# Performance work log

Measured on AMD Instinct MI355X. Metric: run time of the kernel, lower is better.

## Reference

```python
import jax, jax.numpy as jnp
import numpy as np

TEMP_UPDATE = 1e-05
EPS = 1e-12  # torch F.normalize eps


def _l2norm(x, axis):
    n = jnp.sqrt(jnp.sum(x * x, axis=axis, keepdims=True))
    return x / jnp.maximum(n, EPS)


def setup_inputs() -> dict:
    key = jax.random.key(0)
    k1, k2 = jax.random.split(key)
    query = jax.random.normal(k1, (64, 256, 512), dtype=jnp.float32)
    keys = jax.random.normal(k2, (2048, 512), dtype=jnp.float32)
    return {"query": query, "keys": keys}


def reference(query, keys):
    bs, t, d = query.shape
    m = keys.shape[0]
    # F.normalize(query, dim=2)
    q = _l2norm(query, axis=2)
    qr = q.reshape(bs * t, d)                      # [N, d]
    score = qr @ keys.T                            # [N, m]
    score_query = jax.nn.softmax(score, axis=0)    # softmax over queries per slot
    score_memory = jax.nn.softmax(score, axis=1)   # softmax over slots per query
    # topk(1) over memory dim -> argmax slot per query
    g = jnp.argmax(score_memory, axis=1)           # [N] int
    col_max = jnp.max(score_query, axis=0)         # [m]
    # weight per query: score_query[n, g_n] / max(score_query[:, g_n])
    w = jnp.take_along_axis(score_query, g[:, None], axis=1)[:, 0] / col_max[g]
    # fused scatter-add replacing the per-slot python loop
    query_update = jax.ops.segment_sum(w[:, None] * qr, g, num_segments=m)  # [m, d]
    updated = _l2norm(TEMP_UPDATE * query_update + keys, axis=1)
    return jax.lax.stop_gradient(updated)  # original returns .detach()
```

## Files before the change

kernel.cpp:

```cpp
#include <hip/hip_runtime.h>
#include <math.h>

#define N_Q     16384
#define DDIM    512
#define M_SLOTS 2048
#define EPSN    1e-12f
#define TEMPU   1e-5f
#define KSCALE  25.4f
#define QSCALE  127.0f
#define INV_S   (1.0f / (127.0f * 25.4f))
#define NZBLK   73
#define BCAP    32

typedef unsigned int u32;
typedef unsigned long long u64;
typedef __attribute__((ext_vector_type(4))) int i32x4;

__device__ __forceinline__ void gld_lds16(const void* g, void* l) {
    __builtin_amdgcn_global_load_lds(
        (const __attribute__((address_space(1))) u32*)(g),
        (__attribute__((address_space(3))) u32*)(l), 16, 0, 0);
}
__device__ __forceinline__ float block_reduce_sum_128(float v, float* sred, int t) {
    #pragma unroll
    for (int o = 32; o > 0; o >>= 1) v += __shfl_down(v, o, 64);
    if ((t & 63) == 0) sred[t >> 6] = v;
    __syncthreads();
    return sred[0] + sred[1];
}
__device__ __forceinline__ char q8(float x, float s) {
    int v = __float2int_rn(x * s);
    v = v < -127 ? -127 : (v > 127 ? 127 : v);
    return (char)v;
}

__global__ __launch_bounds__(128) void k_prep(const float* __restrict__ q,
                                              const float* __restrict__ keys,
                                              char* __restrict__ qi8,
                                              char* __restrict__ ki8,
                                              float4* __restrict__ zbase) {
    __shared__ float sred[2];
    int b = blockIdx.x;
    int t = threadIdx.x;
    if (b < N_Q) {
        float4 v = ((const float4*)(q + (size_t)b * DDIM))[t];
        float ss = v.x * v.x + v.y * v.y + v.z * v.z + v.w * v.w;
        ss = block_reduce_sum_128(ss, sred, t);
        float s = QSCALE / fmaxf(sqrtf(ss), EPSN);
        char4 o;
        o.x = q8(v.x, s);
        o.y = q8(v.y, s);
        o.z = q8(v.z, s);
        o.w = q8(v.w, s);
        ((char4*)(qi8 + (size_t)b * DDIM))[t] = o;
    } else if (b < N_Q + M_SLOTS) {
        int r = b - N_Q;
        float4 v = ((const float4*)(keys + (size_t)r * DDIM))[t];
        char4 o;
        o.x = q8(v.x, KSCALE);
        o.y = q8(v.y, KSCALE);
        o.z = q8(v.z, KSCALE);
        o.w = q8(v.w, KSCALE);
        ((char4*)(ki8 + (size_t)r * DDIM))[t] = o;
    } else {
        int idx = (b - (N_Q + M_SLOTS)) * 128 + t;
        zbase[idx] = make_float4(0.f, 0.f, 0.f, 0.f);
    }
}

__global__ __launch_bounds__(256) void k_score(const char* __restrict__ qi8,
                                               const char* __restrict__ ki8,
                                               u64* __restrict__ rowpack,
                                               u32* __restrict__ colmax) {
    __shared__ char sA[3][128 * 64];
    __shared__ char sB[3][128 * 64];

    int t = threadIdx.x;
    int lane = t & 63;
    int wid = t >> 6;
    int wrow = wid >> 1;
    int wcol = wid & 1;
    int lr = lane & 15;
    int kc = lane >> 4;

    int n0 = blockIdx.y * 128;
    int j0 = blockIdx.x * 128;

    int srow = t >> 2;
    int scolB = (t & 3) * 16;

    const char* gA0 = qi8 + (size_t)(n0 + srow) * DDIM + scolB;
    const char* gA1 = qi8 + (size_t)(n0 + 64 + srow) * DDIM + scolB;
    const char* gB0 = ki8 + (size_t)(j0 + srow) * DDIM + scolB;
    const char* gB1 = ki8 + (size_t)(j0 + 64 + srow) * DDIM + scolB;

    i32x4 acc[4][4] = {};

#define STAGE(buf, k0)  do {                                   \
        gld_lds16(gA0 + (k0), &sA[buf][t * 16]);               \
        gld_lds16(gA1 + (k0), &sA[buf][4096 + t * 16]);        \
        gld_lds16(gB0 + (k0), &sB[buf][t * 16]);               \
        gld_lds16(gB1 + (k0), &sB[buf][4096 + t * 16]);        \
    } while (0)

    STAGE(0, 0);
    STAGE(1, 64);
    asm volatile("s_waitcnt vmcnt(4)" ::: "memory");
    __builtin_amdgcn_s_barrier();
    __builtin_amdgcn_sched_barrier(0);

    #pragma unroll
    for (int kt = 0; kt < 8; ++kt) {
        const int cur = kt % 3;
        if (kt < 6) STAGE((kt + 2) % 3, (kt + 2) * 64);

        i32x4 a[4], b[4];
        #pragma unroll
        for (int i = 0; i < 4; ++i)
            a[i] = *(const i32x4*)&sA[cur][(wrow * 64 + i * 16 + lr) * 64 + kc * 16];
        #pragma unroll
        for (int j = 0; j < 4; ++j)
            b[j] = *(const i32x4*)&sB[cur][(wcol * 64 + j * 16 + lr) * 64 + kc * 16];
        #pragma unroll
        for (int i = 0; i < 4; ++i)
            #pragma unroll
            for (int j = 0; j < 4; ++j)
                acc[i][j] = __builtin_amdgcn_mfma_i32_16x16x64_i8(a[i], b[j], acc[i][j], 0, 0, 0);

        if (kt < 6)       asm volatile("s_waitcnt vmcnt(4)" ::: "memory");
        else if (kt == 6) asm volatile("s_waitcnt vmcnt(0)" ::: "memory");
        if (kt < 7) {
            __builtin_amdgcn_s_barrier();
            __builtin_amdgcn_sched_barrier(0);
        }
    }
#undef STAGE

    #pragma unroll
    for (int i = 0; i < 4; ++i) {
        #pragma unroll
        for (int r = 0; r < 4; ++r) {
            int v = acc[i][0][r];
            int c = j0 + wcol * 64 + lr;
            #pragma unroll
            for (int j = 1; j < 4; ++j) {
                int vj = acc[i][j][r];
                int cj = j0 + wcol * 64 + j * 16 + lr;
                if (vj > v) { v = vj; c = cj; }
            }
            #pragma unroll
            for (int off = 1; off < 16; off <<= 1) {
                int ov = __shfl_xor(v, off, 64);
                int oc = __shfl_xor(c, off, 64);
                if (ov > v || (ov == v && oc < c)) { v = ov; c = oc; }
            }
            if (lr == 0) {
                int grow = n0 + wrow * 64 + i * 16 + kc * 4 + r;
                u64 pk = ((u64)(u32)(v ^ 0x80000000) << 32) | (u64)(~(u32)c);
                atomicMax(rowpack + grow, pk);
            }
        }
    }
    #pragma unroll
    for (int j = 0; j < 4; ++j) {
        int m = acc[0][j][0];
        #pragma unroll
        for (int i = 0; i < 4; ++i)
            #pragma unroll
            for (int r = 0; r < 4; ++r) m = max(m, acc[i][j][r]);
        m = max(m, __shfl_xor(m, 16, 64));
        m = max(m, __shfl_xor(m, 32, 64));
        if (kc == 0) atomicMax(colmax + j0 + wcol * 64 + j * 16 + lr,
                               (u32)m ^ 0x80000000u);
    }
}

__global__ __launch_bounds__(256) void k_fill(const u64* __restrict__ rowpack,
                                              const u32* __restrict__ colmax,
                                              u32* __restrict__ cur,
                                              u32* __restrict__ bperm,
                                              float* __restrict__ bw,
                                              u32* __restrict__ ovf_cnt,
                                              u32* __restrict__ ovf_n,
                                              float* __restrict__ ovf_w) {
    int n = blockIdx.x * 256 + threadIdx.x;
    u64 p = rowpack[n];
    int vi = (int)(((u32)(p >> 32)) ^ 0x80000000u);
    int g = (int)(~(u32)(p & 0xFFFFFFFFull));
    int cm = (int)(colmax[g] ^ 0x80000000u);
    float w = expf((float)(vi - cm) * INV_S);
    u32 pos = atomicAdd(cur + g, 1u);
    if (pos < BCAP) {
        bperm[g * BCAP + pos] = (u32)n;
        bw[g * BCAP + pos] = w;
    } else {
        u32 o = atomicAdd(ovf_cnt, 1u);
        ovf_n[o] = ((u32)g << 16) | (u32)n;
        ovf_w[o] = w;
    }
}

__global__ __launch_bounds__(128) void k_gather_final(const char* __restrict__ qi8,
                                                      const u32* __restrict__ cur,
                                                      const u32* __restrict__ bperm,
                                                      const float* __restrict__ bw,
                                                      const u32* __restrict__ ovf_cnt,
                                                      const u32* __restrict__ ovf_n,
                                                      const float* __restrict__ ovf_w,
                                                      const float* __restrict__ keys,
                                                      float* __restrict__ out) {
    __shared__ float sred[2];
    int j = blockIdx.x;
    int t = threadIdx.x;
    u32 c = cur[j];
    u32 cnt = c < BCAP ? c : BCAP;
    float ax = 0.f, ay = 0.f, az = 0.f, aw = 0.f;
    for (u32 i = 0; i < cnt; ++i) {
        u32 n = bperm[j * BCAP + i];
        float wq = bw[j * BCAP + i] * (1.0f / 127.0f);
        char4 q4 = ((const char4*)(qi8 + (size_t)n * DDIM))[t];
        ax = fmaf(wq, (float)q4.x, ax);
        ay = fmaf(wq, (float)q4.y, ay);
        az = fmaf(wq, (float)q4.z, az);
        aw = fmaf(wq, (float)q4.w, aw);
    }
    if (c > BCAP) {
        u32 oc = *ovf_cnt;
        for (u32 i = 0; i < oc; ++i) {
            u32 e = ovf_n[i];
            if ((e >> 16) == (u32)j) {
                u32 n = e & 0xFFFFu;
                float wq = ovf_w[i] * (1.0f / 127.0f);
                char4 q4 = ((const char4*)(qi8 + (size_t)n * DDIM))[t];
                ax = fmaf(wq, (float)q4.x, ax);
                ay = fmaf(wq, (float)q4.y, ay);
                az = fmaf(wq, (float)q4.z, az);
                aw = fmaf(wq, (float)q4.w, aw);
            }
        }
    }
    float4 k4 = ((const float4*)(keys + (size_t)j * DDIM))[t];
    float4 v;
    v.x = fmaf(TEMPU, ax, k4.x);
    v.y = fmaf(TEMPU, ay, k4.y);
    v.z = fmaf(TEMPU, az, k4.z);
    v.w = fmaf(TEMPU, aw, k4.w);
    float ss = v.x * v.x + v.y * v.y + v.z * v.z + v.w * v.w;
    ss = block_reduce_sum_128(ss, sred, t);
    float inv = 1.0f / fmaxf(sqrtf(ss), EPSN);
    v.x *= inv; v.y *= inv; v.z *= inv; v.w *= inv;
    ((float4*)(out + (size_t)j * DDIM))[t] = v;
}

extern "C" void kernel_launch(void* const* d_in, const int* in_sizes, int n_in,
                              void* d_out, int out_size, void* d_ws, size_t ws_size,
                              hipStream_t stream) {
    const float* query = (const float*)d_in[0];
    const float* keys  = (const float*)d_in[1];
    float* out = (float*)d_out;

    char* ws = (char*)d_ws;
    const size_t OFF_QI8   = 0;
    const size_t OFF_ROW   = 8388608;
    const size_t OFF_CMAX  = OFF_ROW + 131072;
    const size_t OFF_CUR   = OFF_CMAX + 8192;
    const size_t OFF_OVFC  = OFF_CUR + 8192;
    const size_t OFF_BPERM = OFF_OVFC + 2048;
    const size_t OFF_BW    = OFF_BPERM + 262144;
    const size_t OFF_OVFN  = OFF_BW + 262144;
    const size_t OFF_OVFW  = OFF_OVFN + 65536;
    const size_t OFF_KI8   = OFF_OVFW + 65536;

    char*   qi8    = ws + OFF_QI8;
    u64*    rowpack= (u64*)(ws + OFF_ROW);
    u32*    cmax   = (u32*)(ws + OFF_CMAX);
    u32*    cur    = (u32*)(ws + OFF_CUR);
    u32*    ovfc   = (u32*)(ws + OFF_OVFC);
    u32*    bperm  = (u32*)(ws + OFF_BPERM);
    float*  bw     = (float*)(ws + OFF_BW);
    u32*    ovfn   = (u32*)(ws + OFF_OVFN);
    float*  ovfw   = (float*)(ws + OFF_OVFW);
    char*   ki8    = ws + OFF_KI8;

    k_prep<<<N_Q + M_SLOTS + NZBLK, 128, 0, stream>>>(query, keys, qi8, ki8,
                                                      (float4*)(ws + OFF_ROW));

    dim3 g2(M_SLOTS / 128, N_Q / 128);
    k_score<<<g2, 256, 0, stream>>>(qi8, ki8, rowpack, cmax);

    k_fill<<<N_Q / 256, 256, 0, stream>>>(rowpack, cmax, cur, bperm, bw,
                                          ovfc, ovfn, ovfw);
    k_gather_final<<<M_SLOTS, 128, 0, stream>>>(qi8, cur, bperm, bw,
                                                ovfc, ovfn, ovfw, keys, out);
}
```

Baseline: 72.19 us.

## Fuse slot bucketing into score kernel via per-row completion counters

```diff
diff --git a/kernel.cpp b/kernel.cpp
--- a/kernel.cpp
+++ b/kernel.cpp
@@ -9,8 +9,9 @@
 #define KSCALE  25.4f
 #define QSCALE  127.0f
 #define INV_S   (1.0f / (127.0f * 25.4f))
-#define NZBLK   73
 #define BCAP    32
+#define NROWB   4608
+#define NZF     13440
 
 typedef unsigned int u32;
 typedef unsigned long long u64;
@@ -34,44 +35,50 @@
     return (char)v;
 }
 
-__global__ __launch_bounds__(128) void k_prep(const float* __restrict__ q,
+__global__ __launch_bounds__(256) void k_prep(const float* __restrict__ q,
                                               const float* __restrict__ keys,
                                               char* __restrict__ qi8,
                                               char* __restrict__ ki8,
                                               float4* __restrict__ zbase) {
-    __shared__ float sred[2];
     int b = blockIdx.x;
     int t = threadIdx.x;
-    if (b < N_Q) {
-        float4 v = ((const float4*)(q + (size_t)b * DDIM))[t];
-        float ss = v.x * v.x + v.y * v.y + v.z * v.z + v.w * v.w;
-        ss = block_reduce_sum_128(ss, sred, t);
-        float s = QSCALE / fmaxf(sqrtf(ss), EPSN);
-        char4 o;
-        o.x = q8(v.x, s);
-        o.y = q8(v.y, s);
-        o.z = q8(v.z, s);
-        o.w = q8(v.w, s);
-        ((char4*)(qi8 + (size_t)b * DDIM))[t] = o;
-    } else if (b < N_Q + M_SLOTS) {
-        int r = b - N_Q;
-        float4 v = ((const float4*)(keys + (size_t)r * DDIM))[t];
-        char4 o;
-        o.x = q8(v.x, KSCALE);
-        o.y = q8(v.y, KSCALE);
-        o.z = q8(v.z, KSCALE);
-        o.w = q8(v.w, KSCALE);
-        ((char4*)(ki8 + (size_t)r * DDIM))[t] = o;
+    if (b < NROWB) {
+        int lane = t & 63;
+        int row = b * 4 + (t >> 6);
+        bool isq = row < N_Q;
+        const float* src = isq ? q + (size_t)row * DDIM
+                               : keys + (size_t)(row - N_Q) * DDIM;
+        float4 v0 = ((const float4*)src)[lane];
+        float4 v1 = ((const float4*)src)[lane + 64];
+        float ss = v0.x * v0.x + v0.y * v0.y + v0.z * v0.z + v0.w * v0.w
+                 + v1.x * v1.x + v1.y * v1.y + v1.z * v1.z + v1.w * v1.w;
+        #pragma unroll
+        for (int o = 32; o > 0; o >>= 1) ss += __shfl_xor(ss, o, 64);
+        float s = isq ? QSCALE / fmaxf(sqrtf(ss), EPSN) : KSCALE;
+        char4 o0, o1;
+        o0.x = q8(v0.x, s); o0.y = q8(v0.y, s); o0.z = q8(v0.z, s); o0.w = q8(v0.w, s);
+        o1.x = q8(v1.x, s); o1.y = q8(v1.y, s); o1.z = q8(v1.z, s); o1.w = q8(v1.w, s);
+        char* dst = isq ? qi8 + (size_t)row * DDIM
+                        : ki8 + (size_t)(row - N_Q) * DDIM;
+        ((char4*)dst)[lane] = o0;
+        ((char4*)dst)[lane + 64] = o1;
     } else {
-        int idx = (b - (N_Q + M_SLOTS)) * 128 + t;
-        zbase[idx] = make_float4(0.f, 0.f, 0.f, 0.f);
+        int idx = (b - NROWB) * 256 + t;
+        if (idx < NZF) zbase[idx] = make_float4(0.f, 0.f, 0.f, 0.f);
     }
 }
 
 __global__ __launch_bounds__(256) void k_score(const char* __restrict__ qi8,
                                                const char* __restrict__ ki8,
                                                u64* __restrict__ rowpack,
-                                               u32* __restrict__ colmax) {
+                                               u32* __restrict__ colmax,
+                                               u32* __restrict__ done,
+                                               u32* __restrict__ cur,
+                                               u32* __restrict__ bperm,
+                                               int* __restrict__ bvi,
+                                               u32* __restrict__ ovf_cnt,
+                                               u32* __restrict__ ovf_n,
+                                               int* __restrict__ ovf_vi) {
     __shared__ char sA[3][128 * 64];
     __shared__ char sB[3][128 * 64];
 
@@ -111,16 +118,16 @@
 
     #pragma unroll
     for (int kt = 0; kt < 8; ++kt) {
-        const int cur = kt % 3;
+        const int cb = kt % 3;
         if (kt < 6) STAGE((kt + 2) % 3, (kt + 2) * 64);
 
         i32x4 a[4], b[4];
         #pragma unroll
         for (int i = 0; i < 4; ++i)
-            a[i] = *(const i32x4*)&sA[cur][(wrow * 64 + i * 16 + lr) * 64 + kc * 16];
+            a[i] = *(const i32x4*)&sA[cb][(wrow * 64 + i * 16 + lr) * 64 + kc * 16];
         #pragma unroll
         for (int j = 0; j < 4; ++j)
-            b[j] = *(const i32x4*)&sB[cur][(wcol * 64 + j * 16 + lr) * 64 + kc * 16];
+            b[j] = *(const i32x4*)&sB[cb][(wcol * 64 + j * 16 + lr) * 64 + kc * 16];
         #pragma unroll
         for (int i = 0; i < 4; ++i)
             #pragma unroll
@@ -173,51 +180,55 @@
         if (kc == 0) atomicMax(colmax + j0 + wcol * 64 + j * 16 + lr,
                                (u32)m ^ 0x80000000u);
     }
-}
-
-__global__ __launch_bounds__(256) void k_fill(const u64* __restrict__ rowpack,
-                                              const u32* __restrict__ colmax,
-                                              u32* __restrict__ cur,
-                                              u32* __restrict__ bperm,
-                                              float* __restrict__ bw,
-                                              u32* __restrict__ ovf_cnt,
-                                              u32* __restrict__ ovf_n,
-                                              float* __restrict__ ovf_w) {
-    int n = blockIdx.x * 256 + threadIdx.x;
-    u64 p = rowpack[n];
-    int vi = (int)(((u32)(p >> 32)) ^ 0x80000000u);
-    int g = (int)(~(u32)(p & 0xFFFFFFFFull));
-    int cm = (int)(colmax[g] ^ 0x80000000u);
-    float w = expf((float)(vi - cm) * INV_S);
-    u32 pos = atomicAdd(cur + g, 1u);
-    if (pos < BCAP) {
-        bperm[g * BCAP + pos] = (u32)n;
-        bw[g * BCAP + pos] = w;
-    } else {
-        u32 o = atomicAdd(ovf_cnt, 1u);
-        ovf_n[o] = ((u32)g << 16) | (u32)n;
-        ovf_w[o] = w;
+
+    if (lr == 0) {
+        __threadfence();
+        #pragma unroll
+        for (int i = 0; i < 4; ++i) {
+            #pragma unroll
+            for (int r = 0; r < 4; ++r) {
+                int grow = n0 + wrow * 64 + i * 16 + kc * 4 + r;
+                u32 d = atomicAdd(done + grow, 1u);
+                if (d == 15u) {
+                    __threadfence();
+                    u64 p = atomicMax(rowpack + grow, 0ull);
+                    int vi = (int)(((u32)(p >> 32)) ^ 0x80000000u);
+                    int g  = (int)(~(u32)(p & 0xFFFFFFFFull));
+                    u32 pos = atomicAdd(cur + g, 1u);
+                    if (pos < BCAP) {
+                        bperm[g * BCAP + pos] = (u32)grow;
+                        bvi[g * BCAP + pos] = vi;
+                    } else {
+                        u32 o = atomicAdd(ovf_cnt, 1u);
+                        ovf_n[o] = ((u32)g << 16) | (u32)grow;
+                        ovf_vi[o] = vi;
+                    }
+                }
+            }
+        }
     }
 }
 
 __global__ __launch_bounds__(128) void k_gather_final(const char* __restrict__ qi8,
+                                                      const u32* __restrict__ colmax,
                                                       const u32* __restrict__ cur,
                                                       const u32* __restrict__ bperm,
-                                                      const float* __restrict__ bw,
+                                                      const int* __restrict__ bvi,
                                                       const u32* __restrict__ ovf_cnt,
                                                       const u32* __restrict__ ovf_n,
-                                                      const float* __restrict__ ovf_w,
+                                                      const int* __restrict__ ovf_vi,
                                                       const float* __restrict__ keys,
                                                       float* __restrict__ out) {
     __shared__ float sred[2];
     int j = blockIdx.x;
     int t = threadIdx.x;
+    int cm = (int)(colmax[j] ^ 0x80000000u);
     u32 c = cur[j];
     u32 cnt = c < BCAP ? c : BCAP;
     float ax = 0.f, ay = 0.f, az = 0.f, aw = 0.f;
     for (u32 i = 0; i < cnt; ++i) {
         u32 n = bperm[j * BCAP + i];
-        float wq = bw[j * BCAP + i] * (1.0f / 127.0f);
+        float wq = expf((float)(bvi[j * BCAP + i] - cm) * INV_S) * (1.0f / 127.0f);
         char4 q4 = ((const char4*)(qi8 + (size_t)n * DDIM))[t];
         ax = fmaf(wq, (float)q4.x, ax);
         ay = fmaf(wq, (float)q4.y, ay);
@@ -230,7 +241,7 @@
             u32 e = ovf_n[i];
             if ((e >> 16) == (u32)j) {
                 u32 n = e & 0xFFFFu;
-                float wq = ovf_w[i] * (1.0f / 127.0f);
+                float wq = expf((float)(ovf_vi[i] - cm) * INV_S) * (1.0f / 127.0f);
                 char4 q4 = ((const char4*)(qi8 + (size_t)n * DDIM))[t];
                 ax = fmaf(wq, (float)q4.x, ax);
                 ay = fmaf(wq, (float)q4.y, ay);
@@ -265,31 +276,32 @@
     const size_t OFF_CMAX  = OFF_ROW + 131072;
     const size_t OFF_CUR   = OFF_CMAX + 8192;
     const size_t OFF_OVFC  = OFF_CUR + 8192;
-    const size_t OFF_BPERM = OFF_OVFC + 2048;
-    const size_t OFF_BW    = OFF_BPERM + 262144;
-    const size_t OFF_OVFN  = OFF_BW + 262144;
-    const size_t OFF_OVFW  = OFF_OVFN + 65536;
-    const size_t OFF_KI8   = OFF_OVFW + 65536;
+    const size_t OFF_DONE  = OFF_OVFC + 2048;
+    const size_t OFF_BPERM = OFF_DONE + 65536;
+    const size_t OFF_BVI   = OFF_BPERM + 262144;
+    const size_t OFF_OVFN  = OFF_BVI + 262144;
+    const size_t OFF_OVFVI = OFF_OVFN + 65536;
+    const size_t OFF_KI8   = OFF_OVFVI + 65536;
 
     char*   qi8    = ws + OFF_QI8;
     u64*    rowpack= (u64*)(ws + OFF_ROW);
     u32*    cmax   = (u32*)(ws + OFF_CMAX);
     u32*    cur    = (u32*)(ws + OFF_CUR);
     u32*    ovfc   = (u32*)(ws + OFF_OVFC);
+    u32*    done   = (u32*)(ws + OFF_DONE);
     u32*    bperm  = (u32*)(ws + OFF_BPERM);
-    float*  bw     = (float*)(ws + OFF_BW);
+    int*    bvi    = (int*)(ws + OFF_BVI);
     u32*    ovfn   = (u32*)(ws + OFF_OVFN);
-    float*  ovfw   = (float*)(ws + OFF_OVFW);
+    int*    ovfvi  = (int*)(ws + OFF_OVFVI);
     char*   ki8    = ws + OFF_KI8;
 
-    k_prep<<<N_Q + M_SLOTS + NZBLK, 128, 0, stream>>>(query, keys, qi8, ki8,
-                                                      (float4*)(ws + OFF_ROW));
+    k_prep<<<NROWB + (NZF + 255) / 256, 256, 0, stream>>>(query, keys, qi8, ki8,
+                                                          (float4*)(ws + OFF_ROW));
 
     dim3 g2(M_SLOTS / 128, N_Q / 128);
-    k_score<<<g2, 256, 0, stream>>>(qi8, ki8, rowpack, cmax);
-
-    k_fill<<<N_Q / 256, 256, 0, stream>>>(rowpack, cmax, cur, bperm, bw,
-                                          ovfc, ovfn, ovfw);
-    k_gather_final<<<M_SLOTS, 128, 0, stream>>>(qi8, cur, bperm, bw,
-                                                ovfc, ovfn, ovfw, keys, out);
-}
+    k_score<<<g2, 256, 0, stream>>>(qi8, ki8, rowpack, cmax, done, cur,
+                                    bperm, bvi, ovfc, ovfn, ovfvi);
+
+    k_gather_final<<<M_SLOTS, 128, 0, stream>>>(qi8, cmax, cur, bperm, bvi,
+                                                ovfc, ovfn, ovfvi, keys, out);
+}
```

Measured after the change: 281.1 us. 289% more time.
